# Performance work log

Measured on AMD Instinct MI355X. Metric: run time of the kernel, lower is better.

## Reference

```python
import jax, jax.numpy as jnp
import numpy as np

ROUTINGS = 3


def squash(v):
    # squash along last axis: v/|v| * |v|^2/(1+|v|^2)
    norm = jnp.linalg.norm(v, axis=-1, keepdims=True)
    ns = norm * norm
    return v / norm * (ns / (1.0 + ns))


def setup_inputs() -> dict:
    key = jax.random.key(0)
    k1, k2 = jax.random.split(key)
    B, N, I, D, Din = 256, 10, 1152, 16, 8
    inputs = jax.random.normal(k1, (B, I, Din), dtype=jnp.float32)
    # glorot-uniform-ish init for W [N, I, D, Din]
    limit = np.sqrt(6.0 / (D + Din)).astype(np.float32)
    W = jax.random.uniform(k2, (N, I, D, Din), dtype=jnp.float32,
                           minval=-limit, maxval=limit)
    return {"inputs": inputs, "W": W}


def reference(inputs, W):
    # inputs: [B, I, Din], W: [N, I, D, Din]
    # u_hat[b,n,i,d] = sum_k W[n,i,d,k] * inputs[b,i,k]  (replaces tf.map_fn)
    u_hat = jnp.einsum('nidk,bik->bnid', W, inputs)  # [B, N, I, D]
    b = jnp.zeros(u_hat.shape[:3], dtype=u_hat.dtype)  # [B, N, I]
    outputs = None
    for r in range(ROUTINGS):
        c = jax.nn.softmax(b, axis=1)  # softmax over output capsules N
        outputs = squash(jnp.einsum('bni,bnid->bnd', c, u_hat))  # [B, N, D]
        if r < ROUTINGS - 1:
            # agreement: a[b,n,i] = <outputs[b,n,:], u_hat[b,n,i,:]>
            b = b + jnp.einsum('bnd,bnid->bni', outputs, u_hat)
    return outputs
```

## Files before the change

kernel.cpp:

```cpp
#include <hip/hip_runtime.h>
#include <hip/hip_bf16.h>
#include <stdint.h>


#define BN 256
#define NN 10
#define NH 5
#define II 1152
#define DD 16
#define KK 8
#define NT 18
#define NP 5

typedef unsigned short ushort_t;
typedef unsigned int uint_t;

__device__ __forceinline__ float bflo(uint_t u) {
    union { uint_t i; float f; } v; v.i = u << 16; return v.f;
}
__device__ __forceinline__ float bfhi(uint_t u) {
    union { uint_t i; float f; } v; v.i = u & 0xffff0000u; return v.f;
}
__device__ __forceinline__ uint_t pkbf(float lo, float hi) {
    __hip_bfloat162 h = __float22bfloat162_rn(make_float2(lo, hi));
    uint_t u; __builtin_memcpy(&u, &h, sizeof(u)); return u;
}

__global__ __launch_bounds__(256) void caps_uhat_s0(const float* __restrict__ xg,
                                                    const float* __restrict__ wg,
                                                    ushort_t* __restrict__ u,
                                                    float* __restrict__ part0,
                                                    int b0, int c4)
{
    __shared__ float wlds[4][2048];
    __shared__ float redn[4][64][2];
    const int tid = threadIdx.x;
    const int lane = tid & 63, wv = tid >> 6;
    const int dq = lane & 3, il = lane >> 2;
    const int nb8 = gridDim.x >> 3;
    const int L   = (blockIdx.x & 7) * nb8 + (blockIdx.x >> 3);
    const int it  = L / (NP * c4);
    const int rem = L - it * (NP * c4);
    const int np  = rem / c4;
    const int bl  = (rem - np * c4) * 4;
    const int n0  = np * 2;
    const int i = it * 64 + wv * 16 + il;

    const bool h0 = (il & 1), h1 = (il >> 1) & 1, h2 = (il >> 2) & 1, h3 = (il >> 3) & 1;
    float* myred = &redn[wv][lane][0];
    float* mylds = &wlds[wv][0];
    const int lrow = lane >> 5, lc = lane & 31;
    const float4* wtile0 = (const float4*)(wg + (size_t)(n0 * II + it * 64 + wv * 16) * (DD * KK));

#define STAGE_W(NNV)                                                         \
    {                                                                        \
        const float4* wt = wtile0 + (size_t)(NNV) * II * 32;                 \
        _Pragma("unroll")                                                    \
        for (int j = 0; j < 8; ++j) {                                        \
            int row = lrow + 2 * j;                                          \
            int chunk = row * 32 + (lc ^ (row & 7));                         \
            __builtin_amdgcn_global_load_lds(                                \
                (const __attribute__((address_space(1))) void*)(wt + chunk), \
                (__attribute__((address_space(3))) void*)(mylds + j * 256),  \
                16, 0, 0);                                                   \
        }                                                                    \
    }

    STAGE_W(0);

    float xv[4][8];
#pragma unroll
    for (int bb = 0; bb < 4; ++bb) {
        const float4* xp = (const float4*)(xg + ((size_t)(b0 + bl + bb) * II + i) * KK);
        float4 x0 = xp[0], x1 = xp[1];
        xv[bb][0] = x0.x; xv[bb][1] = x0.y; xv[bb][2] = x0.z; xv[bb][3] = x0.w;
        xv[bb][4] = x1.x; xv[bb][5] = x1.y; xv[bb][6] = x1.z; xv[bb][7] = x1.w;
    }

    auto compute_n = [&](int n, const float4* w, int slot) {
        float s[4][4];
#pragma unroll
        for (int dj = 0; dj < 4; ++dj) {
            float4 wa = w[2 * dj], wb = w[2 * dj + 1];
#pragma unroll
            for (int bb = 0; bb < 4; ++bb) {
                s[bb][dj] = wa.x * xv[bb][0] + wa.y * xv[bb][1]
                          + wa.z * xv[bb][2] + wa.w * xv[bb][3]
                          + wb.x * xv[bb][4] + wb.y * xv[bb][5]
                          + wb.z * xv[bb][6] + wb.w * xv[bb][7];
            }
        }
#pragma unroll
        for (int bb = 0; bb < 4; ++bb) {
            uint2 q;
            q.x = pkbf(s[bb][0], s[bb][1]);
            q.y = pkbf(s[bb][2], s[bb][3]);
            *(uint2*)(u + (((size_t)(bl + bb) * NN + n) * II + i) * DD + dq * 4) = q;
        }
        float v8[8];
#pragma unroll
        for (int k = 0; k < 8; ++k) {
            float a0 = s[(2 * k) >> 2][(2 * k) & 3];
            float a1 = s[(2 * k + 1) >> 2][(2 * k + 1) & 3];
            float give = h0 ? a0 : a1;
            float got  = __shfl_xor(give, 4, 64);
            v8[k] = (h0 ? a1 : a0) + got;
        }
        float v4[4];
#pragma unroll
        for (int k = 0; k < 4; ++k) {
            float a0 = v8[2 * k], a1 = v8[2 * k + 1];
            float give = h1 ? a0 : a1;
            float got  = __shfl_xor(give, 8, 64);
            v4[k] = (h1 ? a1 : a0) + got;
        }
        float v2[2];
#pragma unroll
        for (int k = 0; k < 2; ++k) {
            float a0 = v4[2 * k], a1 = v4[2 * k + 1];
            float give = h2 ? a0 : a1;
            float got  = __shfl_xor(give, 16, 64);
            v2[k] = (h2 ? a1 : a0) + got;
        }
        {
            float a0 = v2[0], a1 = v2[1];
            float give = h3 ? a0 : a1;
            float got  = __shfl_xor(give, 32, 64);
            myred[slot] = (h3 ? a1 : a0) + got;
        }
    };

    float4 w[8];
    asm volatile("s_waitcnt vmcnt(0)" ::: "memory");
#pragma unroll
    for (int jj = 0; jj < 8; ++jj)
        w[jj] = *(const float4*)(mylds + il * 128 + dq * 32 + ((jj ^ (il & 7)) << 2));
    asm volatile("s_waitcnt lgkmcnt(0)" ::: "memory");
    STAGE_W(1);
    compute_n(n0, w, 0);

    asm volatile("s_waitcnt vmcnt(0)" ::: "memory");
#pragma unroll
    for (int jj = 0; jj < 8; ++jj)
        w[jj] = *(const float4*)(mylds + il * 128 + dq * 32 + ((jj ^ (il & 7)) << 2));
    compute_n(n0 + 1, w, 1);
#undef STAGE_W

    __syncthreads();
    if (tid < 128) {
        int bb = tid >> 5, r5 = tid & 31, nn = r5 >> 4, d = r5 & 15;
        int lane2 = ((bb * 4 + (d & 3)) << 2) + (d >> 2);
        float v = redn[0][lane2][nn] + redn[1][lane2][nn]
                + redn[2][lane2][nn] + redn[3][lane2][nn];
        part0[((size_t)(b0 + bl + bb) * NT + it) * 160 + (n0 + nn) * 16 + d] = 0.1f * v;
    }
}

__global__ __launch_bounds__(1024) void caps_route(const ushort_t* __restrict__ u,
                                                   const float* __restrict__ p0,
                                                   float* __restrict__ out, int b0)
{
    __shared__ float red[16][8][20];
    __shared__ float o_s[160];
    __shared__ float s_s[160];
    const int tid = threadIdx.x;
    const int gi = tid >> 3;
    const int gl = tid & 7;
    const int ld = gl & 3, hh = gl >> 2;
    const int wv = tid >> 6, lane = tid & 63;
    const int b = b0 + blockIdx.x;
    const ushort_t* ub = u + (size_t)blockIdx.x * (NN * II * DD);
    const ushort_t* ubh = ub + ((size_t)(hh * NH) * II + gi) * DD + ld * 4;

#define ULOAD(R, S)                                                            \
    _Pragma("unroll")                                                          \
    for (int k = 0; k < NH; ++k)                                               \
        R[k] = *(const uint2*)(ubh + ((size_t)k * II + (S) * 128) * DD);

#define STEP(R)                                                                \
    {                                                                          \
        float p[NH];                                                           \
        _Pragma("unroll")                                                      \
        for (int k = 0; k < NH; ++k) {                                         \
            float4 o4 = *(const float4*)&o_s[hh * 80 + k * 16 + ld * 4];       \
            p[k] = bflo(R[k].x) * o4.x + bfhi(R[k].x) * o4.y                   \
                 + bflo(R[k].y) * o4.z + bfhi(R[k].y) * o4.w;                  \
        }                                                                      \
        float a[NH];                                                           \
        _Pragma("unroll")                                                      \
        for (int k = 0; k < NH; ++k) {                                         \
            float t2 = p[k] + __shfl_xor(p[k], 1, 64);                         \
            a[k] = t2 + __shfl_xor(t2, 2, 64);                                 \
        }                                                                      \
        float mo = fmaxf(fmaxf(fmaxf(a[0], a[1]), fmaxf(a[2], a[3])), a[4]);   \
        float mx = fmaxf(mo, __shfl_xor(mo, 4, 64));                           \
        float c[NH];                                                           \
        _Pragma("unroll")                                                      \
        for (int k = 0; k < NH; ++k) c[k] = __expf(a[k] - mx);                 \
        float so = ((c[0] + c[1]) + (c[2] + c[3])) + c[4];                     \
        float ssum = so + __shfl_xor(so, 4, 64);                               \
        float inv = 1.0f / ssum;                                               \
        _Pragma("unroll")                                                      \
        for (int k = 0; k < NH; ++k) {                                         \
            float w = c[k] * inv;                                              \
            sp[k][0] += w * bflo(R[k].x); sp[k][1] += w * bfhi(R[k].x);        \
            sp[k][2] += w * bflo(R[k].y); sp[k][3] += w * bfhi(R[k].y);        \
        }                                                                      \
    }

#define PASS                                                                   \
    {                                                                          \
        uint2 rA[NH], rB[NH];                                                  \
        ULOAD(rA, 0)                                                           \
        ULOAD(rB, 1)  STEP(rA)                                                 \
        ULOAD(rA, 2)  STEP(rB)                                                 \
        ULOAD(rB, 3)  STEP(rA)                                                 \
        ULOAD(rA, 4)  STEP(rB)                                                 \
        ULOAD(rB, 5)  STEP(rA)                                                 \
        ULOAD(rA, 6)  STEP(rB)                                                 \
        ULOAD(rB, 7)  STEP(rA)                                                 \
        ULOAD(rA, 8)  STEP(rB)                                                 \
        STEP(rA)                                                               \
    }

#define BLOCK_REDUCE(DST)                                                      \
    {                                                                          \
        _Pragma("unroll")                                                      \
        for (int m = 8; m <= 32; m <<= 1)                                      \
            _Pragma("unroll")                                                  \
            for (int k = 0; k < NH; ++k)                                       \
                _Pragma("unroll")                                              \
                for (int j = 0; j < 4; ++j)                                    \
                    sp[k][j] += __shfl_xor(sp[k][j], m, 64);                   \
        if (lane < 8) {                                                        \
            _Pragma("unroll")                                                  \
            for (int k = 0; k < NH; ++k)                                       \
                _Pragma("unroll")                                              \
                for (int j = 0; j < 4; ++j)                                    \
                    red[wv][lane][k * 4 + j] = sp[k][j];                       \
        }                                                                      \
        __syncthreads();                                                       \
        if (tid < 160) {                                                       \
            int n = tid >> 4, d = tid & 15;                                    \
            int h2 = (n >= NH), k2 = n - h2 * NH;                              \
            int l8 = h2 * 4 + (d >> 2), j2 = d & 3;                            \
            float v = 0.f;                                                     \
            _Pragma("unroll")                                                  \
            for (int w = 0; w < 16; ++w) v += red[w][l8][k2 * 4 + j2];         \
            DST[tid] = v;                                                      \
        }                                                                      \
        __syncthreads();                                                       \
    }

    if (tid < 160) {
        float v = 0.f;
#pragma unroll
        for (int t = 0; t < NT; ++t)
            v += p0[((size_t)b * NT + t) * 160 + tid];
        float sq = v * v;
#pragma unroll
        for (int m = 1; m <= 8; m <<= 1) sq += __shfl_xor(sq, m, 64);
        o_s[tid] = v * (sqrtf(sq) / (1.0f + sq));
    }
    __syncthreads();

    float sp[NH][4];
#pragma unroll
    for (int k = 0; k < NH; ++k)
#pragma unroll
        for (int j = 0; j < 4; ++j) sp[k][j] = 0.f;

    PASS
    BLOCK_REDUCE(s_s)

    if (tid < 160) {
        float v = s_s[tid];
        float sq = v * v;
#pragma unroll
        for (int m = 1; m <= 8; m <<= 1) sq += __shfl_xor(sq, m, 64);
        o_s[tid] = o_s[tid] + v * (sqrtf(sq) / (1.0f + sq));
    }
    __syncthreads();

#pragma unroll
    for (int k = 0; k < NH; ++k)
#pragma unroll
        for (int j = 0; j < 4; ++j) sp[k][j] = 0.f;

    PASS
    BLOCK_REDUCE(s_s)

    if (tid < 160) {
        float v = s_s[tid];
        float sq = v * v;
#pragma unroll
        for (int m = 1; m <= 8; m <<= 1) sq += __shfl_xor(sq, m, 64);
        out[(size_t)b * 160 + tid] = v * (sqrtf(sq) / (1.0f + sq));
    }
#undef ULOAD
#undef STEP
#undef PASS
#undef BLOCK_REDUCE
}

extern "C" void kernel_launch(void* const* d_in, const int* in_sizes, int n_in,
                              void* d_out, int out_size, void* d_ws, size_t ws_size,
                              hipStream_t stream)
{
    const float* xg = (const float*)d_in[0];
    const float* wg = (const float*)d_in[1];
    if (n_in >= 2 && in_sizes[0] == NN * II * DD * KK) {
        const float* t = xg; xg = wg; wg = t;
    }
    float* outp = (float*)d_out;

    const size_t perB  = (size_t)NN * II * DD * 2;
    const size_t p0B   = (size_t)BN * NT * 160 * 4;
    size_t extra = p0B;
    size_t avail = (ws_size > extra) ? ws_size - extra : 0;
    int C = 256;
    if (avail < (size_t)256 * perB) {
        C = (int)(avail / perB);
        C &= ~15;
        if (C < 16) C = 16;
    }
    ushort_t* uws = (ushort_t*)d_ws;
    float* part0 = (float*)((char*)d_ws + (size_t)C * perB);

    for (int b0 = 0; b0 < BN; b0 += C) {
        int c = (BN - b0 < C) ? (BN - b0) : C;
        int c4 = c / 4;
        caps_uhat_s0<<<NT * NP * c4, 256, 0, stream>>>(xg, wg, uws, part0, b0, c4);
        caps_route  <<<c, 1024, 0, stream>>>(uws, part0, outp, b0);
    }
}
```

Baseline: 141.0 us.

## Split routing into per-iteration kernels over half-capsule ranges and shrink uhat blocks

Replaces the single 1024-thread-per-batch routing kernel with separate kernels for each routing sweep, each using two blocks per batch element that each cover half of the input capsules and write partial sums, plus a small final squash kernel. The u_hat kernel drops to 64-thread blocks with one wave each, eliminating the shared-memory cross-wave reduction and writing more partial tiles (NT 18→72). The aim is more blocks in flight to fill the GPU with only 256 batch elements. The cost is extra kernel launches, more partial-sum traffic, and re-reading u_hat and the partials across kernels.

```diff
diff --git a/kernel.cpp b/kernel.cpp
--- a/kernel.cpp
+++ b/kernel.cpp
@@ -9,8 +9,9 @@
 #define II 1152
 #define DD 16
 #define KK 8
-#define NT 18
+#define NT 72
 #define NP 5
+#define HLF 576
 
 typedef unsigned short ushort_t;
 typedef unsigned int uint_t;
@@ -26,16 +27,14 @@
     uint_t u; __builtin_memcpy(&u, &h, sizeof(u)); return u;
 }
 
-__global__ __launch_bounds__(256) void caps_uhat_s0(const float* __restrict__ xg,
-                                                    const float* __restrict__ wg,
-                                                    ushort_t* __restrict__ u,
-                                                    float* __restrict__ part0,
-                                                    int b0, int c4)
-{
-    __shared__ float wlds[4][2048];
-    __shared__ float redn[4][64][2];
-    const int tid = threadIdx.x;
-    const int lane = tid & 63, wv = tid >> 6;
+__global__ __launch_bounds__(64) void caps_uhat_s0(const float* __restrict__ xg,
+                                                   const float* __restrict__ wg,
+                                                   ushort_t* __restrict__ u,
+                                                   float* __restrict__ part0,
+                                                   int b0, int c4)
+{
+    __shared__ float wlds[2048];
+    const int lane = threadIdx.x;
     const int dq = lane & 3, il = lane >> 2;
     const int nb8 = gridDim.x >> 3;
     const int L   = (blockIdx.x & 7) * nb8 + (blockIdx.x >> 3);
@@ -44,13 +43,11 @@
     const int np  = rem / c4;
     const int bl  = (rem - np * c4) * 4;
     const int n0  = np * 2;
-    const int i = it * 64 + wv * 16 + il;
+    const int i = it * 16 + il;
 
     const bool h0 = (il & 1), h1 = (il >> 1) & 1, h2 = (il >> 2) & 1, h3 = (il >> 3) & 1;
-    float* myred = &redn[wv][lane][0];
-    float* mylds = &wlds[wv][0];
     const int lrow = lane >> 5, lc = lane & 31;
-    const float4* wtile0 = (const float4*)(wg + (size_t)(n0 * II + it * 64 + wv * 16) * (DD * KK));
+    const float4* wtile0 = (const float4*)(wg + (size_t)(n0 * II + it * 16) * (DD * KK));
 
 #define STAGE_W(NNV)                                                         \
     {                                                                        \
@@ -61,7 +58,7 @@
             int chunk = row * 32 + (lc ^ (row & 7));                         \
             __builtin_amdgcn_global_load_lds(                                \
                 (const __attribute__((address_space(1))) void*)(wt + chunk), \
-                (__attribute__((address_space(3))) void*)(mylds + j * 256),  \
+                (__attribute__((address_space(3))) void*)(wlds + j * 256),   \
                 16, 0, 0);                                                   \
         }                                                                    \
     }
@@ -77,7 +74,7 @@
         xv[bb][4] = x1.x; xv[bb][5] = x1.y; xv[bb][6] = x1.z; xv[bb][7] = x1.w;
     }
 
-    auto compute_n = [&](int n, const float4* w, int slot) {
+    auto compute_n = [&](int n, const float4* w) -> float {
         float s[4][4];
 #pragma unroll
         for (int dj = 0; dj < 4; ++dj) {
@@ -122,62 +119,95 @@
             float got  = __shfl_xor(give, 16, 64);
             v2[k] = (h2 ? a1 : a0) + got;
         }
-        {
-            float a0 = v2[0], a1 = v2[1];
-            float give = h3 ? a0 : a1;
-            float got  = __shfl_xor(give, 32, 64);
-            myred[slot] = (h3 ? a1 : a0) + got;
-        }
+        float a0 = v2[0], a1 = v2[1];
+        float give = h3 ? a0 : a1;
+        float got  = __shfl_xor(give, 32, 64);
+        return (h3 ? a1 : a0) + got;
     };
 
     float4 w[8];
     asm volatile("s_waitcnt vmcnt(0)" ::: "memory");
 #pragma unroll
     for (int jj = 0; jj < 8; ++jj)
-        w[jj] = *(const float4*)(mylds + il * 128 + dq * 32 + ((jj ^ (il & 7)) << 2));
+        w[jj] = *(const float4*)(wlds + il * 128 + dq * 32 + ((jj ^ (il & 7)) << 2));
     asm volatile("s_waitcnt lgkmcnt(0)" ::: "memory");
     STAGE_W(1);
-    compute_n(n0, w, 0);
+    float m0 = compute_n(n0, w);
 
     asm volatile("s_waitcnt vmcnt(0)" ::: "memory");
 #pragma unroll
     for (int jj = 0; jj < 8; ++jj)
-        w[jj] = *(const float4*)(mylds + il * 128 + dq * 32 + ((jj ^ (il & 7)) << 2));
-    compute_n(n0 + 1, w, 1);
+        w[jj] = *(const float4*)(wlds + il * 128 + dq * 32 + ((jj ^ (il & 7)) << 2));
+    float m1 = compute_n(n0 + 1, w);
 #undef STAGE_W
 
-    __syncthreads();
-    if (tid < 128) {
-        int bb = tid >> 5, r5 = tid & 31, nn = r5 >> 4, d = r5 & 15;
-        int lane2 = ((bb * 4 + (d & 3)) << 2) + (d >> 2);
-        float v = redn[0][lane2][nn] + redn[1][lane2][nn]
-                + redn[2][lane2][nn] + redn[3][lane2][nn];
-        part0[((size_t)(b0 + bl + bb) * NT + it) * 160 + (n0 + nn) * 16 + d] = 0.1f * v;
-    }
-}
-
-__global__ __launch_bounds__(1024) void caps_route(const ushort_t* __restrict__ u,
-                                                   const float* __restrict__ p0,
-                                                   float* __restrict__ out, int b0)
-{
-    __shared__ float red[16][8][20];
-    __shared__ float o_s[160];
-    __shared__ float s_s[160];
-    const int tid = threadIdx.x;
-    const int gi = tid >> 3;
-    const int gl = tid & 7;
-    const int ld = gl & 3, hh = gl >> 2;
-    const int wv = tid >> 6, lane = tid & 63;
-    const int b = b0 + blockIdx.x;
-    const ushort_t* ub = u + (size_t)blockIdx.x * (NN * II * DD);
-    const ushort_t* ubh = ub + ((size_t)(hh * NH) * II + gi) * DD + ld * 4;
-
-#define ULOAD(R, S)                                                            \
+    const int bb = il >> 2, dj = il & 3;
+    size_t base = ((size_t)(b0 + bl + bb) * NT + it) * 160 + dq * 4 + dj;
+    part0[base + (size_t)n0 * 16]       = 0.1f * m0;
+    part0[base + (size_t)(n0 + 1) * 16] = 0.1f * m1;
+}
+
+
+#define SWEEP_BODY(OEXPR_SETUP)                                                \
+    __shared__ float red[16][8][20];                                           \
+    __shared__ float o_s[160];                                                 \
+    const int tid = threadIdx.x;                                               \
+    const int gi = tid >> 3, gl = tid & 7;                                     \
+    const int ld = gl & 3, hh = gl >> 2;                                       \
+    const int wv = tid >> 6, lane = tid & 63;                                  \
+    const int cb = blockIdx.x >> 1, h = blockIdx.x & 1;                        \
+    const int b = b0 + cb;                                                     \
+    const ushort_t* ub = u + (size_t)cb * (NN * II * DD);                      \
+    const ushort_t* ubh = ub + (size_t)(hh * NH) * II * DD + ld * 4;           \
+    const int itail = h * HLF + 512 + (gi & 63);                               \
+    const float tmask = (gi < 64) ? 1.f : 0.f;                                 \
+    OEXPR_SETUP                                                                \
+    __syncthreads();                                                           \
+    float sp[NH][4];                                                           \
     _Pragma("unroll")                                                          \
     for (int k = 0; k < NH; ++k)                                               \
-        R[k] = *(const uint2*)(ubh + ((size_t)k * II + (S) * 128) * DD);
-
-#define STEP(R)                                                                \
+        _Pragma("unroll")                                                      \
+        for (int j = 0; j < 4; ++j) sp[k][j] = 0.f;                            \
+    {                                                                          \
+        uint2 rA[NH], rB[NH];                                                  \
+        ULOADI(rA, h * HLF + 0 * 128 + gi)                                     \
+        ULOADI(rB, h * HLF + 1 * 128 + gi)  STEP(rA, 1.f)                      \
+        ULOADI(rA, h * HLF + 2 * 128 + gi)  STEP(rB, 1.f)                      \
+        ULOADI(rB, h * HLF + 3 * 128 + gi)  STEP(rA, 1.f)                      \
+        ULOADI(rA, itail)                   STEP(rB, 1.f)                      \
+        STEP(rA, tmask)                                                        \
+    }                                                                          \
+    _Pragma("unroll")                                                          \
+    for (int m = 8; m <= 32; m <<= 1)                                          \
+        _Pragma("unroll")                                                      \
+        for (int k = 0; k < NH; ++k)                                           \
+            _Pragma("unroll")                                                  \
+            for (int j = 0; j < 4; ++j)                                        \
+                sp[k][j] += __shfl_xor(sp[k][j], m, 64);                       \
+    if (lane < 8) {                                                            \
+        _Pragma("unroll")                                                      \
+        for (int k = 0; k < NH; ++k)                                           \
+            _Pragma("unroll")                                                  \
+            for (int j = 0; j < 4; ++j)                                        \
+                red[wv][lane][k * 4 + j] = sp[k][j];                           \
+    }                                                                          \
+    __syncthreads();                                                           \
+    if (tid < 160) {                                                           \
+        int n = tid >> 4, d = tid & 15;                                        \
+        int h2 = (n >= NH), k2 = n - h2 * NH;                                  \
+        int l8 = h2 * 4 + (d >> 2), j2 = d & 3;                                \
+        float v = 0.f;                                                         \
+        _Pragma("unroll")                                                      \
+        for (int w = 0; w < 16; ++w) v += red[w][l8][k2 * 4 + j2];             \
+        pout[(size_t)(cb * 2 + h) * 160 + tid] = v;                            \
+    }
+
+#define ULOADI(R, IV)                                                          \
+    _Pragma("unroll")                                                          \
+    for (int k = 0; k < NH; ++k)                                               \
+        R[k] = *(const uint2*)(ubh + ((size_t)(k * II + (IV))) * DD);
+
+#define STEP(R, MK)                                                            \
     {                                                                          \
         float p[NH];                                                           \
         _Pragma("unroll")                                                      \
@@ -199,7 +229,7 @@
         for (int k = 0; k < NH; ++k) c[k] = __expf(a[k] - mx);                 \
         float so = ((c[0] + c[1]) + (c[2] + c[3])) + c[4];                     \
         float ssum = so + __shfl_xor(so, 4, 64);                               \
-        float inv = 1.0f / ssum;                                               \
+        float inv = (MK) / ssum;                                               \
         _Pragma("unroll")                                                      \
         for (int k = 0; k < NH; ++k) {                                         \
             float w = c[k] * inv;                                              \
@@ -208,99 +238,60 @@
         }                                                                      \
     }
 
-#define PASS                                                                   \
-    {                                                                          \
-        uint2 rA[NH], rB[NH];                                                  \
-        ULOAD(rA, 0)                                                           \
-        ULOAD(rB, 1)  STEP(rA)                                                 \
-        ULOAD(rA, 2)  STEP(rB)                                                 \
-        ULOAD(rB, 3)  STEP(rA)                                                 \
-        ULOAD(rA, 4)  STEP(rB)                                                 \
-        ULOAD(rB, 5)  STEP(rA)                                                 \
-        ULOAD(rA, 6)  STEP(rB)                                                 \
-        ULOAD(rB, 7)  STEP(rA)                                                 \
-        ULOAD(rA, 8)  STEP(rB)                                                 \
-        STEP(rA)                                                               \
-    }
-
-#define BLOCK_REDUCE(DST)                                                      \
-    {                                                                          \
-        _Pragma("unroll")                                                      \
-        for (int m = 8; m <= 32; m <<= 1)                                      \
-            _Pragma("unroll")                                                  \
-            for (int k = 0; k < NH; ++k)                                       \
-                _Pragma("unroll")                                              \
-                for (int j = 0; j < 4; ++j)                                    \
-                    sp[k][j] += __shfl_xor(sp[k][j], m, 64);                   \
-        if (lane < 8) {                                                        \
-            _Pragma("unroll")                                                  \
-            for (int k = 0; k < NH; ++k)                                       \
-                _Pragma("unroll")                                              \
-                for (int j = 0; j < 4; ++j)                                    \
-                    red[wv][lane][k * 4 + j] = sp[k][j];                       \
-        }                                                                      \
-        __syncthreads();                                                       \
-        if (tid < 160) {                                                       \
-            int n = tid >> 4, d = tid & 15;                                    \
-            int h2 = (n >= NH), k2 = n - h2 * NH;                              \
-            int l8 = h2 * 4 + (d >> 2), j2 = d & 3;                            \
-            float v = 0.f;                                                     \
-            _Pragma("unroll")                                                  \
-            for (int w = 0; w < 16; ++w) v += red[w][l8][k2 * 4 + j2];         \
-            DST[tid] = v;                                                      \
-        }                                                                      \
-        __syncthreads();                                                       \
-    }
-
-    if (tid < 160) {
-        float v = 0.f;
-#pragma unroll
-        for (int t = 0; t < NT; ++t)
-            v += p0[((size_t)b * NT + t) * 160 + tid];
+#define O1_SETUP                                                               \
+    if (tid < 160) {                                                           \
+        float v = 0.f;                                                         \
+        for (int t = 0; t < NT; ++t)                                           \
+            v += p0[((size_t)b * NT + t) * 160 + tid];                         \
+        float sq = v * v;                                                      \
+        _Pragma("unroll")                                                      \
+        for (int m = 1; m <= 8; m <<= 1) sq += __shfl_xor(sq, m, 64);          \
+        o_s[tid] = v * (sqrtf(sq) / (1.0f + sq));                              \
+    }
+
+#define O2_SETUP                                                               \
+    if (tid < 160) {                                                           \
+        float v = 0.f;                                                         \
+        for (int t = 0; t < NT; ++t)                                           \
+            v += p0[((size_t)b * NT + t) * 160 + tid];                         \
+        float sq = v * v;                                                      \
+        _Pragma("unroll")                                                      \
+        for (int m = 1; m <= 8; m <<= 1) sq += __shfl_xor(sq, m, 64);          \
+        float o = v * (sqrtf(sq) / (1.0f + sq));                               \
+        float v1 = p1[(size_t)b * 320 + tid] + p1[(size_t)b * 320 + 160 + tid];\
+        float sq1 = v1 * v1;                                                   \
+        _Pragma("unroll")                                                      \
+        for (int m = 1; m <= 8; m <<= 1) sq1 += __shfl_xor(sq1, m, 64);        \
+        o_s[tid] = o + v1 * (sqrtf(sq1) / (1.0f + sq1));                       \
+    }
+
+__global__ __launch_bounds__(1024) void caps_s1(const ushort_t* __restrict__ u,
+                                                const float* __restrict__ p0,
+                                                float* __restrict__ pout, int b0)
+{
+    SWEEP_BODY(O1_SETUP)
+}
+
+__global__ __launch_bounds__(1024) void caps_s2(const ushort_t* __restrict__ u,
+                                                const float* __restrict__ p0,
+                                                const float* __restrict__ p1,
+                                                float* __restrict__ pout, int b0)
+{
+    SWEEP_BODY(O2_SETUP)
+}
+
+__global__ __launch_bounds__(192) void caps_out(const float* __restrict__ p2,
+                                                float* __restrict__ out, int b0)
+{
+    const int b = b0 + blockIdx.x;
+    const int t = threadIdx.x;
+    if (t < 160) {
+        float v = p2[(size_t)blockIdx.x * 320 + t] + p2[(size_t)blockIdx.x * 320 + 160 + t];
         float sq = v * v;
 #pragma unroll
         for (int m = 1; m <= 8; m <<= 1) sq += __shfl_xor(sq, m, 64);
-        o_s[tid] = v * (sqrtf(sq) / (1.0f + sq));
-    }
-    __syncthreads();
-
-    float sp[NH][4];
-#pragma unroll
-    for (int k = 0; k < NH; ++k)
-#pragma unroll
-        for (int j = 0; j < 4; ++j) sp[k][j] = 0.f;
-
-    PASS
-    BLOCK_REDUCE(s_s)
-
-    if (tid < 160) {
-        float v = s_s[tid];
-        float sq = v * v;
-#pragma unroll
-        for (int m = 1; m <= 8; m <<= 1) sq += __shfl_xor(sq, m, 64);
-        o_s[tid] = o_s[tid] + v * (sqrtf(sq) / (1.0f + sq));
-    }
-    __syncthreads();
-
-#pragma unroll
-    for (int k = 0; k < NH; ++k)
-#pragma unroll
-        for (int j = 0; j < 4; ++j) sp[k][j] = 0.f;
-
-    PASS
-    BLOCK_REDUCE(s_s)
-
-    if (tid < 160) {
-        float v = s_s[tid];
-        float sq = v * v;
-#pragma unroll
-        for (int m = 1; m <= 8; m <<= 1) sq += __shfl_xor(sq, m, 64);
-        out[(size_t)b * 160 + tid] = v * (sqrtf(sq) / (1.0f + sq));
-    }
-#undef ULOAD
-#undef STEP
-#undef PASS
-#undef BLOCK_REDUCE
+        out[(size_t)b * 160 + t] = v * (sqrtf(sq) / (1.0f + sq));
+    }
 }
 
 extern "C" void kernel_launch(void* const* d_in, const int* in_sizes, int n_in,
@@ -316,7 +307,8 @@
 
     const size_t perB  = (size_t)NN * II * DD * 2;
     const size_t p0B   = (size_t)BN * NT * 160 * 4;
-    size_t extra = p0B;
+    const size_t p12B  = (size_t)BN * 2 * 160 * 4;
+    size_t extra = p0B + 2 * p12B;
     size_t avail = (ws_size > extra) ? ws_size - extra : 0;
     int C = 256;
     if (avail < (size_t)256 * perB) {
@@ -326,11 +318,15 @@
     }
     ushort_t* uws = (ushort_t*)d_ws;
     float* part0 = (float*)((char*)d_ws + (size_t)C * perB);
+    float* part1 = part0 + (size_t)BN * NT * 160;
+    float* part2 = part1 + (size_t)BN * 2 * 160;
 
     for (int b0 = 0; b0 < BN; b0 += C) {
         int c = (BN - b0 < C) ? (BN - b0) : C;
         int c4 = c / 4;
-        caps_uhat_s0<<<NT * NP * c4, 256, 0, stream>>>(xg, wg, uws, part0, b0, c4);
-        caps_route  <<<c, 1024, 0, stream>>>(uws, part0, outp, b0);
-    }
-}
+        caps_uhat_s0<<<NT * NP * c4, 64, 0, stream>>>(xg, wg, uws, part0, b0, c4);
+        caps_s1     <<<c * 2, 1024, 0, stream>>>(uws, part0, part1, b0);
+        caps_s2     <<<c * 2, 1024, 0, stream>>>(uws, part0, part1, part2, b0);
+        caps_out    <<<c, 192, 0, stream>>>(part2, outp, b0);
+    }
+}
```

New measurement: 148.1 us. 5.0% more time.

## Process all ten output capsules per block with double-buffered W staging

Applied to the files above, without the earlier changes.

Each u_hat block now loops over all 10 output capsules instead of 2, so the grid shrinks fivefold and the input x values loaded into registers are reused across all capsules. W tiles are double-buffered in LDS, with the next capsule's tile staged asynchronously while the current one is computed. The final reduction now writes all 160 partial-sum entries per batch row. This raises LDS use to about 64KB plus the reduction buffer, which lowers occupancy, and the grid is much smaller, which may leave CUs underused.

```diff
diff --git a/kernel.cpp b/kernel.cpp
--- a/kernel.cpp
+++ b/kernel.cpp
@@ -10,7 +10,6 @@
 #define DD 16
 #define KK 8
 #define NT 18
-#define NP 5
 
 typedef unsigned short ushort_t;
 typedef unsigned int uint_t;
@@ -32,41 +31,36 @@
                                                     float* __restrict__ part0,
                                                     int b0, int c4)
 {
-    __shared__ float wlds[4][2048];
-    __shared__ float redn[4][64][2];
+    __shared__ float wlds[4][2][2048];
+    __shared__ float redn[4][64][NN];
     const int tid = threadIdx.x;
     const int lane = tid & 63, wv = tid >> 6;
     const int dq = lane & 3, il = lane >> 2;
     const int nb8 = gridDim.x >> 3;
     const int L   = (blockIdx.x & 7) * nb8 + (blockIdx.x >> 3);
-    const int it  = L / (NP * c4);
-    const int rem = L - it * (NP * c4);
-    const int np  = rem / c4;
-    const int bl  = (rem - np * c4) * 4;
-    const int n0  = np * 2;
+    const int it  = L / c4;
+    const int bl  = (L - it * c4) * 4;
     const int i = it * 64 + wv * 16 + il;
 
     const bool h0 = (il & 1), h1 = (il >> 1) & 1, h2 = (il >> 2) & 1, h3 = (il >> 3) & 1;
     float* myred = &redn[wv][lane][0];
-    float* mylds = &wlds[wv][0];
     const int lrow = lane >> 5, lc = lane & 31;
-    const float4* wtile0 = (const float4*)(wg + (size_t)(n0 * II + it * 64 + wv * 16) * (DD * KK));
-
-#define STAGE_W(NNV)                                                         \
-    {                                                                        \
-        const float4* wt = wtile0 + (size_t)(NNV) * II * 32;                 \
-        _Pragma("unroll")                                                    \
-        for (int j = 0; j < 8; ++j) {                                        \
-            int row = lrow + 2 * j;                                          \
-            int chunk = row * 32 + (lc ^ (row & 7));                         \
-            __builtin_amdgcn_global_load_lds(                                \
-                (const __attribute__((address_space(1))) void*)(wt + chunk), \
-                (__attribute__((address_space(3))) void*)(mylds + j * 256),  \
-                16, 0, 0);                                                   \
-        }                                                                    \
-    }
-
-    STAGE_W(0);
+    const float4* wtile0 = (const float4*)(wg + (size_t)(it * 64 + wv * 16) * (DD * KK));
+
+    auto stage_w = [&](int n, float* buf) {
+        const float4* wt = wtile0 + (size_t)n * II * 32;
+#pragma unroll
+        for (int j = 0; j < 8; ++j) {
+            int row = lrow + 2 * j;
+            int chunk = row * 32 + (lc ^ (row & 7));
+            __builtin_amdgcn_global_load_lds(
+                (const __attribute__((address_space(1))) void*)(wt + chunk),
+                (__attribute__((address_space(3))) void*)(buf + j * 256),
+                16, 0, 0);
+        }
+    };
+
+    stage_w(0, &wlds[wv][0][0]);
 
     float xv[4][8];
 #pragma unroll
@@ -77,7 +71,17 @@
         xv[bb][4] = x1.x; xv[bb][5] = x1.y; xv[bb][6] = x1.z; xv[bb][7] = x1.w;
     }
 
-    auto compute_n = [&](int n, const float4* w, int slot) {
+#pragma unroll
+    for (int n = 0; n < NN; ++n) {
+        float* buf = &wlds[wv][n & 1][0];
+        asm volatile("s_waitcnt vmcnt(0)" ::: "memory");
+        float4 w[8];
+#pragma unroll
+        for (int jj = 0; jj < 8; ++jj)
+            w[jj] = *(const float4*)(buf + il * 128 + dq * 32 + ((jj ^ (il & 7)) << 2));
+        asm volatile("s_waitcnt lgkmcnt(0)" ::: "memory");
+        if (n < NN - 1) stage_w(n + 1, &wlds[wv][(n + 1) & 1][0]);
+
         float s[4][4];
 #pragma unroll
         for (int dj = 0; dj < 4; ++dj) {
@@ -126,33 +130,19 @@
             float a0 = v2[0], a1 = v2[1];
             float give = h3 ? a0 : a1;
             float got  = __shfl_xor(give, 32, 64);
-            myred[slot] = (h3 ? a1 : a0) + got;
-        }
-    };
-
-    float4 w[8];
-    asm volatile("s_waitcnt vmcnt(0)" ::: "memory");
-#pragma unroll
-    for (int jj = 0; jj < 8; ++jj)
-        w[jj] = *(const float4*)(mylds + il * 128 + dq * 32 + ((jj ^ (il & 7)) << 2));
-    asm volatile("s_waitcnt lgkmcnt(0)" ::: "memory");
-    STAGE_W(1);
-    compute_n(n0, w, 0);
-
-    asm volatile("s_waitcnt vmcnt(0)" ::: "memory");
-#pragma unroll
-    for (int jj = 0; jj < 8; ++jj)
-        w[jj] = *(const float4*)(mylds + il * 128 + dq * 32 + ((jj ^ (il & 7)) << 2));
-    compute_n(n0 + 1, w, 1);
-#undef STAGE_W
+            myred[n] = (h3 ? a1 : a0) + got;
+        }
+    }
 
     __syncthreads();
-    if (tid < 128) {
-        int bb = tid >> 5, r5 = tid & 31, nn = r5 >> 4, d = r5 & 15;
+#pragma unroll
+    for (int idx = tid; idx < 640; idx += 256) {
+        int bb = idx / 160, r = idx - bb * 160;
+        int n = r >> 4, d = r & 15;
         int lane2 = ((bb * 4 + (d & 3)) << 2) + (d >> 2);
-        float v = redn[0][lane2][nn] + redn[1][lane2][nn]
-                + redn[2][lane2][nn] + redn[3][lane2][nn];
-        part0[((size_t)(b0 + bl + bb) * NT + it) * 160 + (n0 + nn) * 16 + d] = 0.1f * v;
+        float v = redn[0][lane2][n] + redn[1][lane2][n]
+                + redn[2][lane2][n] + redn[3][lane2][n];
+        part0[((size_t)(b0 + bl + bb) * NT + it) * 160 + r] = 0.1f * v;
     }
 }
 
@@ -330,7 +320,7 @@
     for (int b0 = 0; b0 < BN; b0 += C) {
         int c = (BN - b0 < C) ? (BN - b0) : C;
         int c4 = c / 4;
-        caps_uhat_s0<<<NT * NP * c4, 256, 0, stream>>>(xg, wg, uws, part0, b0, c4);
+        caps_uhat_s0<<<NT * c4, 256, 0, stream>>>(xg, wg, uws, part0, b0, c4);
         caps_route  <<<c, 1024, 0, stream>>>(uws, part0, outp, b0);
     }
 }
```

Measured after the change: 146.6 us. 4.0% more time.
